# Optimization experiments

Measured on AMD Instinct MI355X. Metric: run time of the kernel, lower is better.

## Reference

```python
import jax, jax.numpy as jnp
import numpy as np

D_MODEL = 1024
NUM_HEADS = 16
HEAD_DIM = D_MODEL // NUM_HEADS  # 64
ROPE_THETA = 10000.0
SEQ_LEN = 4096
BATCH = 1


def apply_rope(x, positions, theta=ROPE_THETA):
    # x: [b, h, s, d], positions: [s]
    d = x.shape[-1]
    inv_freq = theta ** (-jnp.arange(0, d, 2, dtype=jnp.float32) / d)  # [d/2]
    angles = positions.astype(jnp.float32)[:, None] * inv_freq[None, :]  # [s, d/2]
    cos = jnp.cos(angles)  # [s, d/2]
    sin = jnp.sin(angles)
    x1 = x[..., 0::2]  # [b, h, s, d/2]
    x2 = x[..., 1::2]
    r1 = x1 * cos - x2 * sin
    r2 = x1 * sin + x2 * cos
    # interleave back to [..., d]
    out = jnp.stack([r1, r2], axis=-1).reshape(x.shape)
    return out.astype(x.dtype)


def setup_inputs() -> dict:
    key = jax.random.key(0)
    k_x, k_qkv, k_o = jax.random.split(key, 3)
    scale_in = 1.0 / np.sqrt(D_MODEL)
    return {
        "x": jax.random.normal(k_x, (BATCH, SEQ_LEN, D_MODEL), dtype=jnp.float32),
        "token_positions": jnp.arange(SEQ_LEN, dtype=jnp.int64 if jax.config.jax_enable_x64 else jnp.int32),
        "w_qkv": jax.random.normal(k_qkv, (3 * D_MODEL, D_MODEL), dtype=jnp.float32) * scale_in,
        "w_o": jax.random.normal(k_o, (D_MODEL, D_MODEL), dtype=jnp.float32) * scale_in,
    }


def reference(x, token_positions, w_qkv, w_o):
    b, s, _ = x.shape
    # QKV projection (Linear without bias, weight [out, in])
    x_qkv = jnp.einsum('bsd,ed->bse', x, w_qkv)  # [b, s, 3*d_model]
    # rearrange 'b s (three heads kv) -> three b heads s kv'
    x_qkv = x_qkv.reshape(b, s, 3, NUM_HEADS, HEAD_DIM)
    x_qkv = jnp.transpose(x_qkv, (2, 0, 3, 1, 4))  # [3, b, h, s, d]
    q, k, v = x_qkv[0], x_qkv[1], x_qkv[2]
    q = apply_rope(q, token_positions)
    k = apply_rope(k, token_positions)
    # scaled dot-product attention with causal mask
    scores = jnp.einsum('bhnd,bhmd->bhnm', q, k) / jnp.sqrt(jnp.float32(HEAD_DIM))
    causal = jnp.tril(jnp.ones((s, s), dtype=bool))  # [s, s]
    scores = jnp.where(causal[None, None], scores, jnp.float32(-jnp.inf))
    weights = jax.nn.softmax(scores, axis=-1)
    attn = jnp.einsum('bhnm,bhmd->bhnd', weights, v)  # [b, h, s, d]
    attn = jnp.transpose(attn, (0, 2, 1, 3)).reshape(b, s, NUM_HEADS * HEAD_DIM)
    return jnp.einsum('bsd,ed->bse', attn, w_o)
```

## Files before the change

kernel.cpp:

```cpp
#include <hip/hip_runtime.h>

#define SEQ 4096
#define DMODEL 1024
#define HEADS 16
#define HD 64
#define NQKV 3072

typedef __attribute__((ext_vector_type(8))) __bf16 bf16x8;
typedef __attribute__((ext_vector_type(4))) __bf16 bf16x4;
typedef __attribute__((ext_vector_type(8))) short short8;
typedef __attribute__((ext_vector_type(4))) float f32x4;

__device__ __forceinline__ unsigned short f2bf(float f) {
    unsigned u = __builtin_bit_cast(unsigned, f);
    return (unsigned short)((u + 0x7fffu + ((u >> 16) & 1u)) >> 16);
}
__device__ __forceinline__ float bf2f(unsigned short h) {
    return __builtin_bit_cast(float, (unsigned)h << 16);
}

__device__ __forceinline__ void gload16(const void* g, void* l) {
    __builtin_amdgcn_global_load_lds(
        (const __attribute__((address_space(1))) unsigned int*)g,
        (__attribute__((address_space(3))) unsigned int*)l, 16, 0, 0);
}

__global__ void f2bf_all(const float* __restrict__ x, const float* __restrict__ wqkv,
                         const float* __restrict__ wo, unsigned short* __restrict__ dst) {
    const int N0 = SEQ * DMODEL / 4;
    const int N1 = N0 + NQKV * DMODEL / 4;
    const int NT = N1 + DMODEL * DMODEL / 4;
    int i = blockIdx.x * 256 + threadIdx.x;
    int stride = gridDim.x * 256;
    for (; i < NT; i += stride) {
        const float4* src;
        if (i < N0)      src = reinterpret_cast<const float4*>(x) + i;
        else if (i < N1) src = reinterpret_cast<const float4*>(wqkv) + (i - N0);
        else             src = reinterpret_cast<const float4*>(wo) + (i - N1);
        float4 f = *src;
        ushort4 o;
        o.x = f2bf(f.x); o.y = f2bf(f.y); o.z = f2bf(f.z); o.w = f2bf(f.w);
        reinterpret_cast<ushort4*>(dst)[i] = o;
    }
}

template <int EPI>
__global__ __launch_bounds__(256) void gemm_bt(const unsigned short* __restrict__ A,
                                               const unsigned short* __restrict__ B,
                                               float* __restrict__ outF,
                                               unsigned short* __restrict__ outB,
                                               int M, int N, int K) {
    alignas(16) __shared__ unsigned short a_lds[128 * 32];
    alignas(16) __shared__ unsigned short b_lds[128 * 32];
    const int tid = threadIdx.x;
    const int wave = tid >> 6, lane = tid & 63;
    const int l16 = lane & 15, g = lane >> 4;
    const int wr = wave >> 1, wc = wave & 1;
    const int bm = blockIdx.x, bn = blockIdx.y;

    const int lrow = lane >> 2;
    const int lcol = (lane & 3) * 8;

    const unsigned short* Ag = A + (size_t)(bm * 128 + lrow) * K + lcol;
    const unsigned short* Bg = B + (size_t)(bn * 128 + lrow) * K + lcol;

    f32x4 acc[4][4] = {};

    for (int k0 = 0; k0 < K; k0 += 32) {
#pragma unroll
        for (int j = 0; j < 2; ++j) {
            int chunk = wave * 2 + j;
            gload16(Ag + (size_t)(chunk * 16) * K + k0, a_lds + chunk * 512);
            gload16(Bg + (size_t)(chunk * 16) * K + k0, b_lds + chunk * 512);
        }
        __syncthreads();
        bf16x8 af[4], bfr[4];
#pragma unroll
        for (int m = 0; m < 4; ++m)
            af[m] = *reinterpret_cast<const bf16x8*>(a_lds + (wr * 64 + m * 16 + l16) * 32 + g * 8);
#pragma unroll
        for (int n = 0; n < 4; ++n)
            bfr[n] = *reinterpret_cast<const bf16x8*>(b_lds + (wc * 64 + n * 16 + l16) * 32 + g * 8);
#pragma unroll
        for (int m = 0; m < 4; ++m)
#pragma unroll
            for (int n = 0; n < 4; ++n)
                acc[m][n] = __builtin_amdgcn_mfma_f32_16x16x32_bf16(af[m], bfr[n], acc[m][n], 0, 0, 0);
        __syncthreads();
    }

#pragma unroll
    for (int m = 0; m < 4; ++m)
#pragma unroll
        for (int n = 0; n < 4; ++n)
#pragma unroll
            for (int r = 0; r < 4; ++r) {
                int row = bm * 128 + wr * 64 + m * 16 + g * 4 + r;
                int col = bn * 128 + wc * 64 + n * 16 + l16;
                float v = acc[m][n][r];
                if (EPI == 0) {
                    int part = col >> 10;
                    int hd = col & 1023;
                    int h = hd >> 6, d = hd & 63;
                    outB[(size_t)((part * HEADS + h) * SEQ + row) * HD + d] = f2bf(v);
                } else {
                    outF[(size_t)row * N + col] = v;
                }
            }
}

__global__ __launch_bounds__(256) void rope_kernel(unsigned short* qkv, const int* __restrict__ pos) {
    int idx = blockIdx.x * 256 + threadIdx.x;
    int chunk = idx & 7;
    int row = idx >> 3;
    int s = row & (SEQ - 1);
    int ph = row >> 12;
    float p = (float)pos[s];
    float scale = (ph < HEADS) ? 0.125f * 1.4426950408889634f : 1.0f;
    unsigned short* base = qkv + ((size_t)ph * SEQ + s) * HD + chunk * 8;
    short8 v = *reinterpret_cast<short8*>(base);
    short8 o;
    const float k = -13.287712379549449f / 32.0f;
#pragma unroll
    for (int j = 0; j < 4; ++j) {
        int i = chunk * 4 + j;
        float ang = p * exp2f((float)i * k);
        float sn, cs;
        sincosf(ang, &sn, &cs);
        float x1 = bf2f((unsigned short)v[2 * j]);
        float x2 = bf2f((unsigned short)v[2 * j + 1]);
        o[2 * j]     = (short)f2bf((x1 * cs - x2 * sn) * scale);
        o[2 * j + 1] = (short)f2bf((x1 * sn + x2 * cs) * scale);
    }
    *reinterpret_cast<short8*>(base) = o;
}

__global__ __launch_bounds__(256) void transpose_v(const unsigned short* __restrict__ qkv,
                                                   unsigned short* __restrict__ vt) {
    const int st = blockIdx.x;
    const int h = blockIdx.y;
    __shared__ unsigned short tile[64][72];
    const unsigned short* Vg = qkv + (size_t)((2 * HEADS + h) * SEQ) * HD;
    const int tid = threadIdx.x;
#pragma unroll
    for (int j = 0; j < 2; ++j) {
        int b = (tid + j * 256) * 8;
        int row = b >> 6;
        int col = b & 63;
        short8 v = *reinterpret_cast<const short8*>(Vg + (size_t)(st * 64 + row) * HD + col);
#pragma unroll
        for (int i = 0; i < 8; ++i) tile[row][col + i] = (unsigned short)v[i];
    }
    __syncthreads();
#pragma unroll
    for (int j = 0; j < 2; ++j) {
        int b = (tid + j * 256) * 8;
        int d = b >> 6;
        int sc = b & 63;
        short8 o;
#pragma unroll
        for (int i = 0; i < 8; ++i) o[i] = (short)tile[sc + i][d];
        *reinterpret_cast<short8*>(vt + (size_t)(h * HD + d) * SEQ + st * 64 + sc) = o;
    }
}

__global__ __launch_bounds__(512) void attn_kernel(const unsigned short* __restrict__ qkv,
                                                   const unsigned short* __restrict__ vt,
                                                   unsigned short* __restrict__ attnout) {
    const int bid = blockIdx.x;
    const int xcd = bid & 7;
    const int slt = bid >> 3;
    const int j = slt & 31, half = slt >> 5;
    const int h = xcd * 2 + (j & 1);
    const int qb = half ? (j >> 1) : (31 - (j >> 1));
    const int last = 2 * qb + 1;

    const int tid = threadIdx.x;
    const int wave = tid >> 6, lane = tid & 63;
    const int l16 = lane & 15, g = lane >> 4;

    alignas(16) __shared__ unsigned short k_lds[3][64 * 64];
    alignas(16) __shared__ unsigned short v_lds[3][64 * 64];
    alignas(16) __shared__ unsigned short p_lds[8][16 * 64];

    const unsigned short* Qg = qkv + (size_t)((0 * HEADS + h) * SEQ) * HD;
    const unsigned short* Kg = qkv + (size_t)((1 * HEADS + h) * SEQ) * HD;
    const unsigned short* VTg = vt + (size_t)h * HD * SEQ;

    const int qbase = qb * 128 + wave * 16;
    bf16x8 qf[2];
    qf[0] = *reinterpret_cast<const bf16x8*>(Qg + (size_t)(qbase + l16) * HD + g * 8);
    qf[1] = *reinterpret_cast<const bf16x8*>(Qg + (size_t)(qbase + l16) * HD + 32 + g * 8);

    bf16x8 ones;
#pragma unroll
    for (int j2 = 0; j2 < 8; ++j2) ones[j2] = (__bf16)1.0f;

    f32x4 o_acc[4] = {};
    f32x4 l_acc = {};
    float m_r = -1e30f;

    char* pwave = (char*)p_lds + wave * 2048;
    const int rsw = (l16 & 7) << 4;

    auto STAGE = [&](int b, int kt) {
        int base = wave * 1024;
        int byte = base + lane * 16;
        int row = byte >> 7;
        int c8s = ((byte >> 4) & 7) ^ (row & 7);
        gload16(Kg + (size_t)(kt * 64 + row) * HD + c8s * 8, (char*)k_lds[b] + base);
        gload16(VTg + (size_t)row * SEQ + kt * 64 + c8s * 8, (char*)v_lds[b] + base);
    };

    STAGE(0, 0);
    STAGE(1, 1);

    for (int kt = 0; kt <= last; ++kt) {
        const int cur = kt % 3;
        if (kt < last) asm volatile("s_waitcnt vmcnt(2)" ::: "memory");
        else           asm volatile("s_waitcnt vmcnt(0)" ::: "memory");
        __builtin_amdgcn_s_barrier();
        if (kt + 2 <= last) STAGE((kt + 2) % 3, kt + 2);

        if (kt * 64 > qbase + 15) continue;

        f32x4 s[4] = {};
        __builtin_amdgcn_s_setprio(1);
#pragma unroll
        for (int nt = 0; nt < 4; ++nt) {
            int row = nt * 16 + l16;
#pragma unroll
            for (int kk = 0; kk < 2; ++kk) {
                bf16x8 kf = *reinterpret_cast<const bf16x8*>(
                    (char*)k_lds[cur] + row * 128 + (((kk * 4 + g) << 4) ^ rsw));
                s[nt] = __builtin_amdgcn_mfma_f32_16x16x32_bf16(kf, qf[kk], s[nt], 0, 0, 0);
            }
        }
        __builtin_amdgcn_s_setprio(0);

        if (kt * 64 + 63 > qbase) {
            int qrow = qbase + l16;
#pragma unroll
            for (int nt = 0; nt < 4; ++nt)
#pragma unroll
                for (int r = 0; r < 4; ++r)
                    if (kt * 64 + nt * 16 + g * 4 + r > qrow) s[nt][r] = -1e30f;
        }

        float t0 = fmaxf(fmaxf(s[0][0], s[0][1]), s[0][2]);
        float t1 = fmaxf(fmaxf(s[0][3], s[1][0]), s[1][1]);
        float t2 = fmaxf(fmaxf(s[1][2], s[1][3]), s[2][0]);
        float t3 = fmaxf(fmaxf(s[2][1], s[2][2]), s[2][3]);
        float t4 = fmaxf(fmaxf(s[3][0], s[3][1]), s[3][2]);
        float mx = fmaxf(fmaxf(fmaxf(t0, t1), t2), fmaxf(fmaxf(t3, t4), s[3][3]));
        mx = fmaxf(mx, __shfl_xor(mx, 16));
        mx = fmaxf(mx, __shfl_xor(mx, 32));

        if (__any(mx > m_r + 8.0f)) {
            float mnew = fmaxf(m_r, mx);
            float alpha = __builtin_amdgcn_exp2f(m_r - mnew);
            m_r = mnew;
#pragma unroll
            for (int dt = 0; dt < 4; ++dt)
#pragma unroll
                for (int r = 0; r < 4; ++r) o_acc[dt][r] *= alpha;
            l_acc[0] *= alpha;
        }

#pragma unroll
        for (int nt = 0; nt < 4; ++nt)
#pragma unroll
            for (int r = 0; r < 4; ++r) s[nt][r] = __builtin_amdgcn_exp2f(s[nt][r] - m_r);

#pragma unroll
        for (int nt = 0; nt < 4; ++nt) {
            bf16x4 pb;
#pragma unroll
            for (int r = 0; r < 4; ++r) pb[r] = (__bf16)s[nt][r];
            *reinterpret_cast<bf16x4*>(pwave + l16 * 128 + ((nt * 32 + g * 8) ^ rsw)) = pb;
        }
        bf16x8 pfrag[2];
#pragma unroll
        for (int kk = 0; kk < 2; ++kk)
            pfrag[kk] = *reinterpret_cast<const bf16x8*>(
                pwave + l16 * 128 + (((kk * 4 + g) << 4) ^ rsw));

        __builtin_amdgcn_s_setprio(1);
#pragma unroll
        for (int dt = 0; dt < 4; ++dt) {
            int row = dt * 16 + l16;
#pragma unroll
            for (int kk = 0; kk < 2; ++kk) {
                bf16x8 vf = *reinterpret_cast<const bf16x8*>(
                    (char*)v_lds[cur] + row * 128 + (((kk * 4 + g) << 4) ^ rsw));
                o_acc[dt] = __builtin_amdgcn_mfma_f32_16x16x32_bf16(vf, pfrag[kk], o_acc[dt], 0, 0, 0);
            }
        }
        l_acc = __builtin_amdgcn_mfma_f32_16x16x32_bf16(ones, pfrag[0], l_acc, 0, 0, 0);
        l_acc = __builtin_amdgcn_mfma_f32_16x16x32_bf16(ones, pfrag[1], l_acc, 0, 0, 0);
        __builtin_amdgcn_s_setprio(0);
    }

    float inv = 1.0f / l_acc[0];
    int q = qbase + l16;
#pragma unroll
    for (int dt = 0; dt < 4; ++dt) {
        ushort4 ov;
        ov.x = f2bf(o_acc[dt][0] * inv);
        ov.y = f2bf(o_acc[dt][1] * inv);
        ov.z = f2bf(o_acc[dt][2] * inv);
        ov.w = f2bf(o_acc[dt][3] * inv);
        *reinterpret_cast<ushort4*>(attnout + (size_t)q * DMODEL + h * HD + dt * 16 + g * 4) = ov;
    }
}

extern "C" void kernel_launch(void* const* d_in, const int* in_sizes, int n_in,
                              void* d_out, int out_size, void* d_ws, size_t ws_size,
                              hipStream_t stream) {
    const float* x = (const float*)d_in[0];
    const int* pos = (const int*)d_in[1];
    const float* wqkv = (const float*)d_in[2];
    const float* wo = (const float*)d_in[3];
    float* out = (float*)d_out;

    unsigned short* xb = (unsigned short*)d_ws;
    unsigned short* wqkvb = xb + (size_t)SEQ * DMODEL;
    unsigned short* wob = wqkvb + (size_t)NQKV * DMODEL;
    unsigned short* qkvp = wob + (size_t)DMODEL * DMODEL;
    unsigned short* vt = qkvp + (size_t)3 * HEADS * SEQ * HD;
    unsigned short* attnb = vt + (size_t)HEADS * HD * SEQ;

    f2bf_all<<<2048, 256, 0, stream>>>(x, wqkv, wo, xb);

    dim3 g1(SEQ / 128, NQKV / 128);
    gemm_bt<0><<<g1, 256, 0, stream>>>(xb, wqkvb, nullptr, qkvp, SEQ, NQKV, DMODEL);

    rope_kernel<<<(2 * HEADS * SEQ * 8) / 256, 256, 0, stream>>>(qkvp, pos);
    transpose_v<<<dim3(SEQ / 64, HEADS), 256, 0, stream>>>(qkvp, vt);
    attn_kernel<<<512, 512, 0, stream>>>(qkvp, vt, attnb);

    dim3 g2(SEQ / 128, DMODEL / 128);
    gemm_bt<1><<<g2, 256, 0, stream>>>(attnb, wob, out, nullptr, SEQ, DMODEL, DMODEL);
}
```

Baseline: 163.8 us.

## Double-buffer GEMM LDS tiles and widen attention KV tiles to 128

The GEMM now keeps two LDS buffers and prefetches the next K-slice with global_load_lds while the current one is multiplied. This drops one barrier per step and raises MFMA priority. The attention kernel moves from triple-buffered 64-key tiles to double-buffered 128-key tiles, masking and skipping the second half when it lies past the causal diagonal. This halves the number of loop iterations and barriers, but adds LDS use and register pressure, and leaves only one tile of prefetch in flight.

```diff
diff --git a/kernel.cpp b/kernel.cpp
--- a/kernel.cpp
+++ b/kernel.cpp
@@ -50,8 +50,8 @@
                                                float* __restrict__ outF,
                                                unsigned short* __restrict__ outB,
                                                int M, int N, int K) {
-    alignas(16) __shared__ unsigned short a_lds[128 * 32];
-    alignas(16) __shared__ unsigned short b_lds[128 * 32];
+    alignas(16) __shared__ unsigned short a_lds[2][128 * 32];
+    alignas(16) __shared__ unsigned short b_lds[2][128 * 32];
     const int tid = threadIdx.x;
     const int wave = tid >> 6, lane = tid & 63;
     const int l16 = lane & 15, g = lane >> 4;
@@ -65,28 +65,39 @@
     const unsigned short* Bg = B + (size_t)(bn * 128 + lrow) * K + lcol;
 
     f32x4 acc[4][4] = {};
-
-    for (int k0 = 0; k0 < K; k0 += 32) {
+    const int NS = K / 32;
+
+    auto STAGE = [&](int b, int ks) {
 #pragma unroll
         for (int j = 0; j < 2; ++j) {
             int chunk = wave * 2 + j;
-            gload16(Ag + (size_t)(chunk * 16) * K + k0, a_lds + chunk * 512);
-            gload16(Bg + (size_t)(chunk * 16) * K + k0, b_lds + chunk * 512);
-        }
-        __syncthreads();
+            gload16(Ag + (size_t)(chunk * 16) * K + ks * 32, a_lds[b] + chunk * 512);
+            gload16(Bg + (size_t)(chunk * 16) * K + ks * 32, b_lds[b] + chunk * 512);
+        }
+    };
+
+    STAGE(0, 0);
+
+    for (int ks = 0; ks < NS; ++ks) {
+        const int cur = ks & 1;
+        asm volatile("s_waitcnt vmcnt(0)" ::: "memory");
+        __builtin_amdgcn_s_barrier();
+        if (ks + 1 < NS) STAGE(cur ^ 1, ks + 1);
+
         bf16x8 af[4], bfr[4];
 #pragma unroll
         for (int m = 0; m < 4; ++m)
-            af[m] = *reinterpret_cast<const bf16x8*>(a_lds + (wr * 64 + m * 16 + l16) * 32 + g * 8);
+            af[m] = *reinterpret_cast<const bf16x8*>(a_lds[cur] + (wr * 64 + m * 16 + l16) * 32 + g * 8);
 #pragma unroll
         for (int n = 0; n < 4; ++n)
-            bfr[n] = *reinterpret_cast<const bf16x8*>(b_lds + (wc * 64 + n * 16 + l16) * 32 + g * 8);
+            bfr[n] = *reinterpret_cast<const bf16x8*>(b_lds[cur] + (wc * 64 + n * 16 + l16) * 32 + g * 8);
+        __builtin_amdgcn_s_setprio(1);
 #pragma unroll
         for (int m = 0; m < 4; ++m)
 #pragma unroll
             for (int n = 0; n < 4; ++n)
                 acc[m][n] = __builtin_amdgcn_mfma_f32_16x16x32_bf16(af[m], bfr[n], acc[m][n], 0, 0, 0);
-        __syncthreads();
+        __builtin_amdgcn_s_setprio(0);
     }
 
 #pragma unroll
@@ -170,17 +181,16 @@
     const int bid = blockIdx.x;
     const int xcd = bid & 7;
     const int slt = bid >> 3;
-    const int j = slt & 31, half = slt >> 5;
+    const int j = slt & 31, hlf = slt >> 5;
     const int h = xcd * 2 + (j & 1);
-    const int qb = half ? (j >> 1) : (31 - (j >> 1));
-    const int last = 2 * qb + 1;
+    const int qb = hlf ? (j >> 1) : (31 - (j >> 1));
 
     const int tid = threadIdx.x;
     const int wave = tid >> 6, lane = tid & 63;
     const int l16 = lane & 15, g = lane >> 4;
 
-    alignas(16) __shared__ unsigned short k_lds[3][64 * 64];
-    alignas(16) __shared__ unsigned short v_lds[3][64 * 64];
+    alignas(16) __shared__ unsigned short k_lds[2][128 * 64];
+    alignas(16) __shared__ unsigned short v_lds[2][64 * 128];
     alignas(16) __shared__ unsigned short p_lds[8][16 * 64];
 
     const unsigned short* Qg = qkv + (size_t)((0 * HEADS + h) * SEQ) * HD;
@@ -204,27 +214,30 @@
     const int rsw = (l16 & 7) << 4;
 
     auto STAGE = [&](int b, int kt) {
-        int base = wave * 1024;
-        int byte = base + lane * 16;
-        int row = byte >> 7;
-        int c8s = ((byte >> 4) & 7) ^ (row & 7);
-        gload16(Kg + (size_t)(kt * 64 + row) * HD + c8s * 8, (char*)k_lds[b] + base);
-        gload16(VTg + (size_t)row * SEQ + kt * 64 + c8s * 8, (char*)v_lds[b] + base);
+#pragma unroll
+        for (int i = 0; i < 2; ++i) {
+            int base = wave * 2048 + i * 1024;
+            int byte = base + lane * 16;
+            int krow = byte >> 7;
+            int kc8 = ((byte >> 4) & 7) ^ (krow & 7);
+            gload16(Kg + (size_t)(kt * 128 + krow) * HD + kc8 * 8, (char*)k_lds[b] + base);
+            int vrow = byte >> 8;
+            int vc16 = ((byte >> 4) & 15) ^ (vrow & 7);
+            gload16(VTg + (size_t)vrow * SEQ + kt * 128 + vc16 * 8, (char*)v_lds[b] + base);
+        }
     };
 
     STAGE(0, 0);
-    STAGE(1, 1);
-
-    for (int kt = 0; kt <= last; ++kt) {
-        const int cur = kt % 3;
-        if (kt < last) asm volatile("s_waitcnt vmcnt(2)" ::: "memory");
-        else           asm volatile("s_waitcnt vmcnt(0)" ::: "memory");
+
+    for (int kt = 0; kt <= qb; ++kt) {
+        const int cur = kt & 1;
+        asm volatile("s_waitcnt vmcnt(0)" ::: "memory");
         __builtin_amdgcn_s_barrier();
-        if (kt + 2 <= last) STAGE((kt + 2) % 3, kt + 2);
-
-        if (kt * 64 > qbase + 15) continue;
-
-        f32x4 s[4] = {};
+        if (kt < qb) STAGE(cur ^ 1, kt + 1);
+
+        const bool doB = (kt * 128 + 64) <= (qbase + 15);
+
+        f32x4 s[8] = {};
         __builtin_amdgcn_s_setprio(1);
 #pragma unroll
         for (int nt = 0; nt < 4; ++nt) {
@@ -236,23 +249,40 @@
                 s[nt] = __builtin_amdgcn_mfma_f32_16x16x32_bf16(kf, qf[kk], s[nt], 0, 0, 0);
             }
         }
+        if (doB) {
+#pragma unroll
+            for (int nt = 0; nt < 4; ++nt) {
+                int row = 64 + nt * 16 + l16;
+#pragma unroll
+                for (int kk = 0; kk < 2; ++kk) {
+                    bf16x8 kf = *reinterpret_cast<const bf16x8*>(
+                        (char*)k_lds[cur] + row * 128 + (((kk * 4 + g) << 4) ^ rsw));
+                    s[4 + nt] = __builtin_amdgcn_mfma_f32_16x16x32_bf16(kf, qf[kk], s[4 + nt], 0, 0, 0);
+                }
+            }
+        }
         __builtin_amdgcn_s_setprio(0);
 
-        if (kt * 64 + 63 > qbase) {
+        if (kt * 128 + 127 > qbase) {
             int qrow = qbase + l16;
 #pragma unroll
             for (int nt = 0; nt < 4; ++nt)
 #pragma unroll
-                for (int r = 0; r < 4; ++r)
-                    if (kt * 64 + nt * 16 + g * 4 + r > qrow) s[nt][r] = -1e30f;
-        }
-
-        float t0 = fmaxf(fmaxf(s[0][0], s[0][1]), s[0][2]);
-        float t1 = fmaxf(fmaxf(s[0][3], s[1][0]), s[1][1]);
-        float t2 = fmaxf(fmaxf(s[1][2], s[1][3]), s[2][0]);
-        float t3 = fmaxf(fmaxf(s[2][1], s[2][2]), s[2][3]);
-        float t4 = fmaxf(fmaxf(s[3][0], s[3][1]), s[3][2]);
-        float mx = fmaxf(fmaxf(fmaxf(t0, t1), t2), fmaxf(fmaxf(t3, t4), s[3][3]));
+                for (int r = 0; r < 4; ++r) {
+                    int kv = kt * 128 + nt * 16 + g * 4 + r;
+                    if (kv > qrow) s[nt][r] = -1e30f;
+                    if (kv + 64 > qrow) s[4 + nt][r] = -1e30f;
+                }
+        }
+
+        f32x4 m4;
+#pragma unroll
+        for (int r = 0; r < 4; ++r) {
+            float a = fmaxf(fmaxf(s[0][r], s[1][r]), fmaxf(s[2][r], s[3][r]));
+            float b = fmaxf(fmaxf(s[4][r], s[5][r]), fmaxf(s[6][r], s[7][r]));
+            m4[r] = fmaxf(a, b);
+        }
+        float mx = fmaxf(fmaxf(m4[0], m4[1]), fmaxf(m4[2], m4[3]));
         mx = fmaxf(mx, __shfl_xor(mx, 16));
         mx = fmaxf(mx, __shfl_xor(mx, 32));
 
@@ -268,36 +298,40 @@
         }
 
 #pragma unroll
-        for (int nt = 0; nt < 4; ++nt)
-#pragma unroll
-            for (int r = 0; r < 4; ++r) s[nt][r] = __builtin_amdgcn_exp2f(s[nt][r] - m_r);
-
-#pragma unroll
-        for (int nt = 0; nt < 4; ++nt) {
-            bf16x4 pb;
-#pragma unroll
-            for (int r = 0; r < 4; ++r) pb[r] = (__bf16)s[nt][r];
-            *reinterpret_cast<bf16x4*>(pwave + l16 * 128 + ((nt * 32 + g * 8) ^ rsw)) = pb;
-        }
-        bf16x8 pfrag[2];
-#pragma unroll
-        for (int kk = 0; kk < 2; ++kk)
-            pfrag[kk] = *reinterpret_cast<const bf16x8*>(
-                pwave + l16 * 128 + (((kk * 4 + g) << 4) ^ rsw));
+        for (int i = 0; i < 8; ++i)
+#pragma unroll
+            for (int r = 0; r < 4; ++r) s[i][r] = __builtin_amdgcn_exp2f(s[i][r] - m_r);
 
         __builtin_amdgcn_s_setprio(1);
 #pragma unroll
-        for (int dt = 0; dt < 4; ++dt) {
-            int row = dt * 16 + l16;
-#pragma unroll
-            for (int kk = 0; kk < 2; ++kk) {
-                bf16x8 vf = *reinterpret_cast<const bf16x8*>(
-                    (char*)v_lds[cur] + row * 128 + (((kk * 4 + g) << 4) ^ rsw));
-                o_acc[dt] = __builtin_amdgcn_mfma_f32_16x16x32_bf16(vf, pfrag[kk], o_acc[dt], 0, 0, 0);
-            }
-        }
-        l_acc = __builtin_amdgcn_mfma_f32_16x16x32_bf16(ones, pfrag[0], l_acc, 0, 0, 0);
-        l_acc = __builtin_amdgcn_mfma_f32_16x16x32_bf16(ones, pfrag[1], l_acc, 0, 0, 0);
+        for (int h64 = 0; h64 < 2; ++h64) {
+            if (h64 && !doB) break;
+#pragma unroll
+            for (int nt = 0; nt < 4; ++nt) {
+                bf16x4 pb;
+#pragma unroll
+                for (int r = 0; r < 4; ++r) pb[r] = (__bf16)s[h64 * 4 + nt][r];
+                *reinterpret_cast<bf16x4*>(pwave + l16 * 128 + ((nt * 32 + g * 8) ^ rsw)) = pb;
+            }
+            bf16x8 pfrag[2];
+#pragma unroll
+            for (int kk = 0; kk < 2; ++kk)
+                pfrag[kk] = *reinterpret_cast<const bf16x8*>(
+                    pwave + l16 * 128 + (((kk * 4 + g) << 4) ^ rsw));
+
+#pragma unroll
+            for (int dt = 0; dt < 4; ++dt) {
+                int row = dt * 16 + l16;
+#pragma unroll
+                for (int kk = 0; kk < 2; ++kk) {
+                    bf16x8 vf = *reinterpret_cast<const bf16x8*>(
+                        (char*)v_lds[cur] + row * 256 + ((h64 * 128 + kk * 64 + g * 16) ^ rsw));
+                    o_acc[dt] = __builtin_amdgcn_mfma_f32_16x16x32_bf16(vf, pfrag[kk], o_acc[dt], 0, 0, 0);
+                }
+            }
+            l_acc = __builtin_amdgcn_mfma_f32_16x16x32_bf16(ones, pfrag[0], l_acc, 0, 0, 0);
+            l_acc = __builtin_amdgcn_mfma_f32_16x16x32_bf16(ones, pfrag[1], l_acc, 0, 0, 0);
+        }
         __builtin_amdgcn_s_setprio(0);
     }
 
```

New measurement: 149.3 us (median of 2 runs). 8.9% less time.
